# Performance work log

Measured on AMD Instinct MI355X. Metric: run time of the kernel, lower is better.

## Reference

```python
import jax, jax.numpy as jnp
import numpy as np

N_STEPS = 5
N_ETYPES = 4
N_GRAPHS = 64
HEADS = 2
N, E, D = 50000, 600000, 128
C = 32


def setup_inputs() -> dict:
    key = jax.random.key(0)
    ks = jax.random.split(key, 24)
    s = 0.08  # param scale to keep activations well-conditioned
    return {
        "in_feat1": jax.random.normal(ks[0], (N, D), jnp.float32),
        "in_feat2": jax.random.normal(ks[1], (N, D), jnp.float32),
        "src1": jax.random.randint(ks[2], (E,), 0, N, jnp.int32),
        "dst1": jax.random.randint(ks[3], (E,), 0, N, jnp.int32),
        "etype1": jax.random.randint(ks[4], (E,), 0, N_ETYPES, jnp.int32),
        "gid1": jnp.sort(jax.random.randint(ks[5], (N,), 0, N_GRAPHS, jnp.int32)),
        "src2": jax.random.randint(ks[6], (E,), 0, N, jnp.int32),
        "dst2": jax.random.randint(ks[7], (E,), 0, N, jnp.int32),
        "etype2": jax.random.randint(ks[8], (E,), 0, N_ETYPES, jnp.int32),
        "gid2": jnp.sort(jax.random.randint(ks[9], (N,), 0, N_GRAPHS, jnp.int32)),
        "W_et": jax.random.normal(ks[10], (N_ETYPES, D, D), jnp.float32) * s,
        "b_et": jax.random.normal(ks[11], (N_ETYPES, D), jnp.float32) * s,
        "W_ih": jax.random.normal(ks[12], (3 * D, D), jnp.float32) * s,
        "W_hh": jax.random.normal(ks[13], (3 * D, D), jnp.float32) * s,
        "b_ih": jax.random.normal(ks[14], (3 * D,), jnp.float32) * s,
        "b_hh": jax.random.normal(ks[15], (3 * D,), jnp.float32) * s,
        "W_fc": jax.random.normal(ks[16], (HEADS * D, D), jnp.float32) * s,
        "attn_l": jax.random.normal(ks[17], (HEADS, D), jnp.float32) * s,
        "attn_r": jax.random.normal(ks[18], (HEADS, D), jnp.float32) * s,
        "gat_bias": jax.random.normal(ks[19], (HEADS * D,), jnp.float32) * s,
        "W_cls": jax.random.normal(ks[20], (C, D), jnp.float32) * s,
        "b_cls": jax.random.normal(ks[21], (C,), jnp.float32) * s,
    }


def _ggann(feat, src, dst, etype, gid,
           W_et, b_et, W_ih, W_hh, b_ih, b_hh,
           W_fc, attn_l, attn_r, gat_bias, W_cls, b_cls):
    n = feat.shape[0]
    h = feat  # in_feats == out_feats -> no zero-padding needed
    # ---- GatedGraphConv: n_steps of per-etype message passing + GRU ----
    for _ in range(N_STEPS):
        # per-etype linear on all nodes: [K, N, D]
        t = jnp.einsum('kod,nd->kno', W_et, h) + b_et[:, None, :]
        msg = t[etype, src]                         # [E, D] gather by (etype, src)
        a = jax.ops.segment_sum(msg, dst, num_segments=n)  # [N, D]
        # GRUCell(a, h)
        gi = a @ W_ih.T + b_ih                      # [N, 3D]
        gh = h @ W_hh.T + b_hh
        i_r, i_z, i_n = jnp.split(gi, 3, axis=1)
        h_r, h_z, h_n = jnp.split(gh, 3, axis=1)
        r = jax.nn.sigmoid(i_r + h_r)
        z = jax.nn.sigmoid(i_z + h_z)
        nn_ = jnp.tanh(i_n + r * h_n)
        h = (1.0 - z) * nn_ + z * h
    # F.normalize (L2 over dim=1) then sigmoid
    h = h / jnp.maximum(jnp.linalg.norm(h, axis=1, keepdims=True), 1e-12)
    h = jax.nn.sigmoid(h)
    # ---- GATConv (num_heads=2) ----
    zft = (h @ W_fc.T).reshape(n, HEADS, D)         # [N, H, D]
    el = jnp.sum(zft * attn_l[None], axis=-1)       # [N, H]
    er = jnp.sum(zft * attn_r[None], axis=-1)
    e = jax.nn.leaky_relu(el[src] + er[dst], 0.2)   # [E, H]
    m = jax.ops.segment_max(e, dst, num_segments=n)
    ex = jnp.exp(e - m[dst])
    den = jax.ops.segment_sum(ex, dst, num_segments=n)
    alpha = ex / den[dst]                           # edge softmax per dst, per head
    rst = jax.ops.segment_sum(alpha[:, :, None] * zft[src], dst, num_segments=n)
    rst = rst + gat_bias.reshape(1, HEADS, D)
    h = jax.nn.relu(rst)                            # [N, H, D] (dropout = eval identity)
    # ---- mean_nodes per graph + classify ----
    sums = jax.ops.segment_sum(h, gid, num_segments=N_GRAPHS)      # [B, H, D]
    cnt = jax.ops.segment_sum(jnp.ones((n, 1, 1), h.dtype), gid, num_segments=N_GRAPHS)
    hg = sums / jnp.maximum(cnt, 1.0)
    return hg @ W_cls.T + b_cls                     # [B, H, C]


def reference(in_feat1, in_feat2, src1, dst1, etype1, gid1,
              src2, dst2, etype2, gid2,
              W_et, b_et, W_ih, W_hh, b_ih, b_hh,
              W_fc, attn_l, attn_r, gat_bias, W_cls, b_cls):
    params = (W_et, b_et, W_ih, W_hh, b_ih, b_hh,
              W_fc, attn_l, attn_r, gat_bias, W_cls, b_cls)
    h1 = _ggann(in_feat1, src1, dst1, etype1, gid1, *params)  # [B, H, C]
    h2 = _ggann(in_feat2, src2, dst2, etype2, gid2, *params)
    # F.pairwise_distance(p=2, eps=1e-6) over last dim -> [B, H]
    dist = jnp.linalg.norm(h1 - h2 + 1e-6, axis=-1)
    return jax.nn.softmax(dist, axis=1)             # softmax over the 2 heads
```

## Files before the change

kernel.cpp:

```cpp
#include <hip/hip_runtime.h>
#include <math.h>

#define D 128
#define NG 64
#define NG2 128
#define NSTEPS 5

using short8 = __attribute__((ext_vector_type(8))) short;
using f32x4  = __attribute__((ext_vector_type(4))) float;
using f32x2  = __attribute__((ext_vector_type(2))) float;

__device__ __forceinline__ float sigf(float x) {
  float e = __expf(-fabsf(x));
  float inv = __fdividef(1.f, 1.f + e);
  return x >= 0.f ? inv : e * inv;
}
__device__ __forceinline__ float tanhf_fast(float x) {
  float e = __expf(-2.f * fabsf(x));
  float r = (1.f - e) * __fdividef(1.f, 1.f + e);
  return x >= 0.f ? r : -r;
}
__device__ __forceinline__ float lrelu(float x) { return x > 0.f ? x : 0.2f * x; }
__device__ __forceinline__ short f2bf(float x) {
  unsigned u = __float_as_uint(x);
  u += 0x7fff + ((u >> 16) & 1);
  return (short)(u >> 16);
}
__device__ __forceinline__ unsigned pk2(float x, float y) {
  return ((unsigned)(unsigned short)f2bf(y) << 16) | (unsigned short)f2bf(x);
}
__device__ __forceinline__ float bflo(unsigned v) { return __uint_as_float(v << 16); }
__device__ __forceinline__ float bfhi(unsigned v) { return __uint_as_float(v & 0xffff0000u); }
__device__ __forceinline__ float bf2f(short s) {
  return __uint_as_float(((unsigned)(unsigned short)s) << 16);
}
__device__ __forceinline__ unsigned char f2fp8(float x) {
  int p = __builtin_amdgcn_cvt_pk_fp8_f32(x, x, 0, false);
  return (unsigned char)(p & 0xff);
}

__global__ void k_init(const float* __restrict__ f1, const float* __restrict__ f2,
                       short* __restrict__ hb, int Nd4) {
  int tot = 2 * Nd4;
  for (int i = blockIdx.x * blockDim.x + threadIdx.x; i < tot; i += gridDim.x * blockDim.x) {
    float4 v = (i < Nd4) ? ((const float4*)f1)[i] : ((const float4*)f2)[i - Nd4];
    ((uint2*)hb)[i] = make_uint2(pk2(v.x, v.y), pk2(v.z, v.w));
  }
}

__global__ void k_pack(const float* __restrict__ W, short* __restrict__ P, int NC) {
  int n = NC * 128;
  for (int i = blockIdx.x * blockDim.x + threadIdx.x; i < n; i += gridDim.x * blockDim.x) {
    int j = i & 7;
    int lane = (i >> 3) & 63;
    int kt = (i >> 9) & 3;
    int nt = i >> 11;
    int c = nt * 16 + (lane & 15);
    int k = kt * 32 + ((lane >> 4) << 3) + j;
    P[i] = f2bf(W[c * 128 + k]);
  }
}

__global__ void k_packA512(const float* __restrict__ W_et, short* __restrict__ P) {
  int n = 128 * 512;
  for (int i = blockIdx.x * blockDim.x + threadIdx.x; i < n; i += gridDim.x * blockDim.x) {
    int j = i & 7;
    int lane = (i >> 3) & 63;
    int kt = (i >> 9) & 15;
    int nt = i >> 13;
    int c = nt * 16 + (lane & 15);
    int k = kt * 32 + ((lane >> 4) << 3) + j;
    P[i] = f2bf(W_et[(k >> 7) * 16384 + c * 128 + (k & 127)]);
  }
}

__global__ void k_hist(const int* __restrict__ dst1, const int* __restrict__ dst2,
                       int E, int N, int* __restrict__ deg) {
  for (int e = blockIdx.x * blockDim.x + threadIdx.x; e < 2 * E; e += gridDim.x * blockDim.x) {
    int d = (e < E) ? dst1[e] : dst2[e - E] + N;
    atomicAdd(&deg[d], 1);
  }
}

__global__ __launch_bounds__(256) void k_scan_a(const int* __restrict__ deg, int n,
                                                int* __restrict__ bsum) {
  int base = blockIdx.x * 1024 + threadIdx.x * 4;
  int s = 0;
  if (base + 3 < n) {
    int4 v = *(const int4*)(deg + base);
    s = v.x + v.y + v.z + v.w;
  } else {
    for (int k = 0; k < 4; ++k) if (base + k < n) s += deg[base + k];
  }
  #pragma unroll
  for (int off = 32; off; off >>= 1) s += __shfl_xor(s, off);
  __shared__ int ws[4];
  if ((threadIdx.x & 63) == 0) ws[threadIdx.x >> 6] = s;
  __syncthreads();
  if (threadIdx.x == 0) bsum[blockIdx.x] = ws[0] + ws[1] + ws[2] + ws[3];
}

__global__ __launch_bounds__(1024) void k_scan_b(const int* __restrict__ bsum,
                                                 int* __restrict__ boffs, int nb) {
  int tid = threadIdx.x;
  int v = (tid < nb) ? bsum[tid] : 0;
  int lane = tid & 63, wv = tid >> 6;
  int x = v;
  #pragma unroll
  for (int off = 1; off < 64; off <<= 1) {
    int y = __shfl_up(x, off);
    if (lane >= off) x += y;
  }
  __shared__ int wsum[16];
  if (lane == 63) wsum[wv] = x;
  __syncthreads();
  if (tid < 16) {
    int u = wsum[tid];
    #pragma unroll
    for (int off = 1; off < 16; off <<= 1) {
      int y = __shfl_up(u, off);
      if (tid >= off) u += y;
    }
    wsum[tid] = u;
  }
  __syncthreads();
  int woff = wv ? wsum[wv - 1] : 0;
  if (tid < nb) boffs[tid] = woff + x - v;
}

__global__ __launch_bounds__(256) void k_scan_c(const int* __restrict__ deg,
    const int* __restrict__ boffs, int* __restrict__ row_ofs,
    int* __restrict__ cursor, int n) {
  int base = blockIdx.x * 1024 + threadIdx.x * 4;
  int v[4] = {0, 0, 0, 0};
  if (base + 3 < n) {
    int4 t = *(const int4*)(deg + base);
    v[0] = t.x; v[1] = t.y; v[2] = t.z; v[3] = t.w;
  } else {
    for (int k = 0; k < 4; ++k) if (base + k < n) v[k] = deg[base + k];
  }
  int s = v[0] + v[1] + v[2] + v[3];
  int lane = threadIdx.x & 63, wv = threadIdx.x >> 6;
  int x = s;
  #pragma unroll
  for (int off = 1; off < 64; off <<= 1) {
    int y = __shfl_up(x, off);
    if (lane >= off) x += y;
  }
  __shared__ int wsum[4];
  if (lane == 63) wsum[wv] = x;
  __syncthreads();
  int woff = 0;
  for (int w = 0; w < wv; ++w) woff += wsum[w];
  int run = boffs[blockIdx.x] + woff + x - s;
  #pragma unroll
  for (int k = 0; k < 4; ++k) {
    int i = base + k;
    if (i < n) {
      cursor[i] = run;
      run += v[k];
      row_ofs[i + 1] = run;
    }
  }
  if (blockIdx.x == 0 && threadIdx.x == 0) row_ofs[0] = 0;
}

__global__ void k_scatter(const int* __restrict__ src1, const int* __restrict__ dst1,
                          const int* __restrict__ ety1, const int* __restrict__ src2,
                          const int* __restrict__ dst2, const int* __restrict__ ety2,
                          int E, int N, int* __restrict__ cursor,
                          int* __restrict__ csr_se) {
  for (int e = blockIdx.x * blockDim.x + threadIdx.x; e < 2 * E; e += gridDim.x * blockDim.x) {
    int s, d, et;
    if (e < E) { s = src1[e]; d = dst1[e]; et = ety1[e]; }
    else { s = src2[e - E] + N; d = dst2[e - E] + N; et = ety2[e - E]; }
    int p = atomicAdd(&cursor[d], 1);
    csr_se[p] = s * 4 + et;
  }
}

__global__ void k_fillgid(const int* __restrict__ gid1, const int* __restrict__ gid2,
                          int N, int* __restrict__ gidc, int* __restrict__ gcnt) {
  __shared__ int cnt[NG2];
  int t = threadIdx.x;
  if (t < NG2) cnt[t] = 0;
  __syncthreads();
  int i = blockIdx.x * 256 + t;
  if (i < 2 * N) {
    int g = (i < N) ? gid1[i] : gid2[i - N] + NG;
    gidc[i] = g;
    atomicAdd(&cnt[g], 1);
  }
  __syncthreads();
  if (t < NG2 && cnt[t]) atomicAdd(&gcnt[t], cnt[t]);
}

__global__ __launch_bounds__(1024) void k_aggemm(const short* __restrict__ hb,
    const int* __restrict__ row_ofs, const int* __restrict__ csr_se,
    const short* __restrict__ WaP, const float* __restrict__ b_et,
    short* __restrict__ ab, int M) {
  __shared__ short Stile[16 * 512];
  __shared__ float lcnt[16][4];
  int tid = threadIdx.x;
  int lane = tid & 63, wave = tid >> 6;
  int row0 = blockIdx.x * 16;

  int li = wave;
  int node = row0 + li;
  float a0x = 0.f, a0y = 0.f, a1x = 0.f, a1y = 0.f;
  float a2x = 0.f, a2y = 0.f, a3x = 0.f, a3y = 0.f;
  int c0 = 0, c1 = 0, c2 = 0, c3 = 0;
  if (node < M) {
    int beg = row_ofs[node], end = row_ofs[node + 1];
    #define ACC(ET, VX, VY) do { \
        if (ET == 0)      { a0x += VX; a0y += VY; ++c0; } \
        else if (ET == 1) { a1x += VX; a1y += VY; ++c1; } \
        else if (ET == 2) { a2x += VX; a2y += VY; ++c2; } \
        else              { a3x += VX; a3y += VY; ++c3; } } while (0)
    for (int base = beg; base < end; base += 64) {
      int nv = end - base; if (nv > 64) nv = 64;
      int r = (lane < nv) ? csr_se[base + lane] : 0;
      int j = 0;
      for (; j + 8 <= nv; j += 8) {
        int rr0 = __builtin_amdgcn_readlane(r, j + 0);
        int rr1 = __builtin_amdgcn_readlane(r, j + 1);
        int rr2 = __builtin_amdgcn_readlane(r, j + 2);
        int rr3 = __builtin_amdgcn_readlane(r, j + 3);
        int rr4 = __builtin_amdgcn_readlane(r, j + 4);
        int rr5 = __builtin_amdgcn_readlane(r, j + 5);
        int rr6 = __builtin_amdgcn_readlane(r, j + 6);
        int rr7 = __builtin_amdgcn_readlane(r, j + 7);
        unsigned v0 = ((const unsigned*)(hb + (size_t)(rr0 >> 2) * 128))[lane];
        unsigned v1 = ((const unsigned*)(hb + (size_t)(rr1 >> 2) * 128))[lane];
        unsigned v2 = ((const unsigned*)(hb + (size_t)(rr2 >> 2) * 128))[lane];
        unsigned v3 = ((const unsigned*)(hb + (size_t)(rr3 >> 2) * 128))[lane];
        unsigned v4 = ((const unsigned*)(hb + (size_t)(rr4 >> 2) * 128))[lane];
        unsigned v5 = ((const unsigned*)(hb + (size_t)(rr5 >> 2) * 128))[lane];
        unsigned v6 = ((const unsigned*)(hb + (size_t)(rr6 >> 2) * 128))[lane];
        unsigned v7 = ((const unsigned*)(hb + (size_t)(rr7 >> 2) * 128))[lane];
        ACC(rr0 & 3, bflo(v0), bfhi(v0));
        ACC(rr1 & 3, bflo(v1), bfhi(v1));
        ACC(rr2 & 3, bflo(v2), bfhi(v2));
        ACC(rr3 & 3, bflo(v3), bfhi(v3));
        ACC(rr4 & 3, bflo(v4), bfhi(v4));
        ACC(rr5 & 3, bflo(v5), bfhi(v5));
        ACC(rr6 & 3, bflo(v6), bfhi(v6));
        ACC(rr7 & 3, bflo(v7), bfhi(v7));
      }
      for (; j + 4 <= nv; j += 4) {
        int rr0 = __builtin_amdgcn_readlane(r, j + 0);
        int rr1 = __builtin_amdgcn_readlane(r, j + 1);
        int rr2 = __builtin_amdgcn_readlane(r, j + 2);
        int rr3 = __builtin_amdgcn_readlane(r, j + 3);
        unsigned v0 = ((const unsigned*)(hb + (size_t)(rr0 >> 2) * 128))[lane];
        unsigned v1 = ((const unsigned*)(hb + (size_t)(rr1 >> 2) * 128))[lane];
        unsigned v2 = ((const unsigned*)(hb + (size_t)(rr2 >> 2) * 128))[lane];
        unsigned v3 = ((const unsigned*)(hb + (size_t)(rr3 >> 2) * 128))[lane];
        ACC(rr0 & 3, bflo(v0), bfhi(v0));
        ACC(rr1 & 3, bflo(v1), bfhi(v1));
        ACC(rr2 & 3, bflo(v2), bfhi(v2));
        ACC(rr3 & 3, bflo(v3), bfhi(v3));
      }
      for (; j < nv; ++j) {
        int rr = __builtin_amdgcn_readlane(r, j);
        unsigned v = ((const unsigned*)(hb + (size_t)(rr >> 2) * 128))[lane];
        ACC(rr & 3, bflo(v), bfhi(v));
      }
    }
    #undef ACC
  }
  {
    int swz = (li & 7) << 4;
    unsigned* ld = (unsigned*)Stile;
    ld[(li * 1024 + ((lane * 4      ) ^ swz)) >> 2] = pk2(a0x, a0y);
    ld[(li * 1024 + ((lane * 4 + 256) ^ swz)) >> 2] = pk2(a1x, a1y);
    ld[(li * 1024 + ((lane * 4 + 512) ^ swz)) >> 2] = pk2(a2x, a2y);
    ld[(li * 1024 + ((lane * 4 + 768) ^ swz)) >> 2] = pk2(a3x, a3y);
    if (lane == 0) {
      lcnt[li][0] = (float)c0; lcnt[li][1] = (float)c1;
      lcnt[li][2] = (float)c2; lcnt[li][3] = (float)c3;
    }
  }
  __syncthreads();

  if (wave < 8) {
    int quad = lane >> 4, l15 = lane & 15;
    int swz = (l15 & 7) << 4;
    int nt = wave;
    f32x4 acc = {0.f, 0.f, 0.f, 0.f};
    #pragma unroll
    for (int kt = 0; kt < 16; ++kt) {
      int boff = l15 * 1024 + ((kt * 64 + quad * 16) ^ swz);
      short8 a = *(const short8*)((const char*)Stile + boff);
      short8 b = *(const short8*)(WaP + (((size_t)(nt * 16 + kt) * 64) + lane) * 8);
      acc = __builtin_amdgcn_mfma_f32_16x16x32_bf16(a, b, acc, 0, 0, 0);
    }
    int c = nt * 16 + l15;
    float be0 = b_et[c], be1 = b_et[128 + c], be2 = b_et[256 + c], be3 = b_et[384 + c];
    #pragma unroll
    for (int reg = 0; reg < 4; ++reg) {
      int lr = quad * 4 + reg;
      int r = row0 + lr;
      if (r < M) {
        float v = acc[reg] + lcnt[lr][0] * be0 + lcnt[lr][1] * be1
                           + lcnt[lr][2] * be2 + lcnt[lr][3] * be3;
        ab[(size_t)r * 128 + c] = f2bf(v);
      }
    }
  }
}

__global__ __launch_bounds__(256) void k_gru_mfma(const short* __restrict__ ab,
    short* __restrict__ hb,
    const short* __restrict__ Pih, const short* __restrict__ Phh,
    const float* __restrict__ b_ih, const float* __restrict__ b_hh, int M) {
  int tid = threadIdx.x;
  int lane = tid & 63, wave = tid >> 6;
  int row0 = blockIdx.x * 128 + wave * 32;
  int quad = lane >> 4, l15 = lane & 15;
  short8 fa[2][4], fh[2][4];
  #pragma unroll
  for (int rt = 0; rt < 2; ++rt) {
    int ar = row0 + rt * 16 + l15; if (ar >= M) ar = M - 1;
    #pragma unroll
    for (int kt = 0; kt < 4; ++kt) {
      fa[rt][kt] = *(const short8*)(ab + (size_t)ar * 128 + kt * 32 + quad * 8);
      fh[rt][kt] = *(const short8*)(hb + (size_t)ar * 128 + kt * 32 + quad * 8);
    }
  }
  for (int nt = 0; nt < 8; ++nt) {
    f32x4 accr[2], accz[2], acci[2], acch[2];
    #pragma unroll
    for (int rt = 0; rt < 2; ++rt) {
      accr[rt] = {0.f,0.f,0.f,0.f}; accz[rt] = {0.f,0.f,0.f,0.f};
      acci[rt] = {0.f,0.f,0.f,0.f}; acch[rt] = {0.f,0.f,0.f,0.f};
    }
    #pragma unroll
    for (int kt = 0; kt < 4; ++kt) {
      size_t li = ((size_t)lane) * 8;
      short8 wr = *(const short8*)(Pih + ((size_t)((nt     ) * 4 + kt) * 64) * 8 + li);
      short8 wz = *(const short8*)(Pih + ((size_t)((nt +  8) * 4 + kt) * 64) * 8 + li);
      short8 wn = *(const short8*)(Pih + ((size_t)((nt + 16) * 4 + kt) * 64) * 8 + li);
      short8 ur = *(const short8*)(Phh + ((size_t)((nt     ) * 4 + kt) * 64) * 8 + li);
      short8 uz = *(const short8*)(Phh + ((size_t)((nt +  8) * 4 + kt) * 64) * 8 + li);
      short8 un = *(const short8*)(Phh + ((size_t)((nt + 16) * 4 + kt) * 64) * 8 + li);
      #pragma unroll
      for (int rt = 0; rt < 2; ++rt) {
        accr[rt] = __builtin_amdgcn_mfma_f32_16x16x32_bf16(fa[rt][kt], wr, accr[rt], 0, 0, 0);
        accr[rt] = __builtin_amdgcn_mfma_f32_16x16x32_bf16(fh[rt][kt], ur, accr[rt], 0, 0, 0);
        accz[rt] = __builtin_amdgcn_mfma_f32_16x16x32_bf16(fa[rt][kt], wz, accz[rt], 0, 0, 0);
        accz[rt] = __builtin_amdgcn_mfma_f32_16x16x32_bf16(fh[rt][kt], uz, accz[rt], 0, 0, 0);
        acci[rt] = __builtin_amdgcn_mfma_f32_16x16x32_bf16(fa[rt][kt], wn, acci[rt], 0, 0, 0);
        acch[rt] = __builtin_amdgcn_mfma_f32_16x16x32_bf16(fh[rt][kt], un, acch[rt], 0, 0, 0);
      }
    }
    int c = nt * 16 + l15;
    float bir = b_ih[c],      bhr = b_hh[c];
    float biz = b_ih[c+128],  bhz = b_hh[c+128];
    float bin_= b_ih[c+256],  bhn = b_hh[c+256];
    #pragma unroll
    for (int rt = 0; rt < 2; ++rt) {
      #pragma unroll
      for (int reg = 0; reg < 4; ++reg) {
        int r = row0 + rt * 16 + quad * 4 + reg;
        if (r < M) {
          float rg = sigf(accr[rt][reg] + bir + bhr);
          float zg = sigf(accz[rt][reg] + biz + bhz);
          float ng = tanhf_fast(acci[rt][reg] + bin_ + rg * (acch[rt][reg] + bhn));
          float hold = bf2f(hb[(size_t)r * 128 + c]);
          float hn2 = (1.f - zg) * ng + zg * hold;
          hb[(size_t)r * 128 + c] = f2bf(hn2);
        }
      }
    }
  }
}

__global__ __launch_bounds__(256) void k_fc_eler(const short* __restrict__ Ab,
    const short* __restrict__ Bp, const float* __restrict__ attn_l,
    const float* __restrict__ attn_r, unsigned char* __restrict__ zq,
    float* __restrict__ el, float* __restrict__ er, int M) {
  int tid = threadIdx.x;
  int lane = tid & 63, wave = tid >> 6;
  int row0 = blockIdx.x * 128 + wave * 32;
  int quad = lane >> 4, l15 = lane & 15;
  short8 af[2][4];
  #pragma unroll
  for (int rt = 0; rt < 2; ++rt) {
    int ar = row0 + rt * 16 + l15; if (ar >= M) ar = M - 1;
    #pragma unroll
    for (int kt = 0; kt < 4; ++kt)
      af[rt][kt] = *(const short8*)(Ab + (size_t)ar * 128 + kt * 32 + quad * 8);
  }
  #pragma unroll
  for (int rt = 0; rt < 2; ++rt) {
    float ss = 0.f;
    #pragma unroll
    for (int kt = 0; kt < 4; ++kt)
      #pragma unroll
      for (int j = 0; j < 8; ++j) {
        float x = bf2f(af[rt][kt][j]);
        ss += x * x;
      }
    ss += __shfl_xor(ss, 16);
    ss += __shfl_xor(ss, 32);
    float inv = 1.f / fmaxf(sqrtf(ss), 1e-12f);
    #pragma unroll
    for (int kt = 0; kt < 4; ++kt)
      #pragma unroll
      for (int j = 0; j < 8; ++j)
        af[rt][kt][j] = f2bf(sigf(bf2f(af[rt][kt][j]) * inv));
  }
  float elp[2][2][4] = {};
  float erp[2][2][4] = {};
  for (int nt = 0; nt < 16; ++nt) {
    f32x4 a0 = {0.f,0.f,0.f,0.f}, a1 = {0.f,0.f,0.f,0.f};
    #pragma unroll
    for (int kt = 0; kt < 4; ++kt) {
      short8 b = *(const short8*)(Bp + (((size_t)(nt * 4 + kt) * 64) + lane) * 8);
      a0 = __builtin_amdgcn_mfma_f32_16x16x32_bf16(af[0][kt], b, a0, 0, 0, 0);
      a1 = __builtin_amdgcn_mfma_f32_16x16x32_bf16(af[1][kt], b, a1, 0, 0, 0);
    }
    int head = nt >> 3;
    int colh = (nt & 7) * 16 + l15;
    float alv = attn_l[head * 128 + colh];
    float arv = attn_r[head * 128 + colh];
    int c = nt * 16 + l15;
    #pragma unroll
    for (int rt = 0; rt < 2; ++rt) {
      f32x4 acc = rt ? a1 : a0;
      #pragma unroll
      for (int reg = 0; reg < 4; ++reg) {
        int r = row0 + rt * 16 + quad * 4 + reg;
        if (r < M) zq[(size_t)r * 256 + c] = f2fp8(acc[reg]);
        elp[rt][head][reg] += acc[reg] * alv;
        erp[rt][head][reg] += acc[reg] * arv;
      }
    }
  }
  #pragma unroll
  for (int off = 1; off < 16; off <<= 1) {
    #pragma unroll
    for (int rt = 0; rt < 2; ++rt)
      #pragma unroll
      for (int h = 0; h < 2; ++h)
        #pragma unroll
        for (int reg = 0; reg < 4; ++reg) {
          elp[rt][h][reg] += __shfl_xor(elp[rt][h][reg], off);
          erp[rt][h][reg] += __shfl_xor(erp[rt][h][reg], off);
        }
  }
  if (l15 == 0) {
    #pragma unroll
    for (int rt = 0; rt < 2; ++rt)
      #pragma unroll
      for (int h = 0; h < 2; ++h)
        #pragma unroll
        for (int reg = 0; reg < 4; ++reg) {
          int r = row0 + rt * 16 + quad * 4 + reg;
          if (r < M) {
            el[r * 2 + h] = elp[rt][h][reg];
            er[r * 2 + h] = erp[rt][h][reg];
          }
        }
  }
}

__global__ __launch_bounds__(256) void k_gat(const unsigned char* __restrict__ zq,
    const float* __restrict__ el, const float* __restrict__ er,
    const int* __restrict__ row_ofs, const int* __restrict__ csr_se,
    const float* __restrict__ gat_bias, short* __restrict__ outb, int N) {
  int node = blockIdx.x * 4 + (threadIdx.x >> 6);
  int lane = threadIdx.x & 63;
  if (node >= N) return;
  int beg = row_ofs[node], end = row_ofs[node + 1];
  float2 ern = ((const float2*)er)[node];
  float l0 = 0.f, l1 = 0.f;
  float4 acc = {0.f, 0.f, 0.f, 0.f};
  int head = lane >> 5;
  for (int base = beg; base < end; base += 64) {
    int nv = end - base; if (nv > 64) nv = 64;
    int sidx = (lane < nv) ? (csr_se[base + lane] >> 2) : 0;
    float p0 = 0.f, p1 = 0.f;
    if (lane < nv) {
      float2 els = ((const float2*)el)[sidx];
      p0 = expf(lrelu(els.x + ern.x));
      p1 = expf(lrelu(els.y + ern.y));
    }
    float t0 = p0, t1 = p1;
    #pragma unroll
    for (int off = 32; off; off >>= 1) { t0 += __shfl_xor(t0, off); t1 += __shfl_xor(t1, off); }
    l0 += t0; l1 += t1;
    int w01 = (int)pk2(p0, p1);
    int j = 0;
    for (; j + 4 <= nv; j += 4) {
      int s0 = __builtin_amdgcn_readlane(sidx, j + 0);
      int s1 = __builtin_amdgcn_readlane(sidx, j + 1);
      int s2 = __builtin_amdgcn_readlane(sidx, j + 2);
      int s3 = __builtin_amdgcn_readlane(sidx, j + 3);
      unsigned w0 = (unsigned)__builtin_amdgcn_readlane(w01, j + 0);
      unsigned w1 = (unsigned)__builtin_amdgcn_readlane(w01, j + 1);
      unsigned w2 = (unsigned)__builtin_amdgcn_readlane(w01, j + 2);
      unsigned w3 = (unsigned)__builtin_amdgcn_readlane(w01, j + 3);
      unsigned z0 = ((const unsigned*)(zq + (size_t)s0 * 256))[lane];
      unsigned z1 = ((const unsigned*)(zq + (size_t)s1 * 256))[lane];
      unsigned z2 = ((const unsigned*)(zq + (size_t)s2 * 256))[lane];
      unsigned z3 = ((const unsigned*)(zq + (size_t)s3 * 256))[lane];
      float f0 = head ? bfhi(w0) : bflo(w0);
      float f1 = head ? bfhi(w1) : bflo(w1);
      float f2 = head ? bfhi(w2) : bflo(w2);
      float f3 = head ? bfhi(w3) : bflo(w3);
      f32x2 lo, hi;
      lo = __builtin_amdgcn_cvt_pk_f32_fp8(z0, false);
      hi = __builtin_amdgcn_cvt_pk_f32_fp8(z0, true);
      acc.x += f0 * lo[0]; acc.y += f0 * lo[1]; acc.z += f0 * hi[0]; acc.w += f0 * hi[1];
      lo = __builtin_amdgcn_cvt_pk_f32_fp8(z1, false);
      hi = __builtin_amdgcn_cvt_pk_f32_fp8(z1, true);
      acc.x += f1 * lo[0]; acc.y += f1 * lo[1]; acc.z += f1 * hi[0]; acc.w += f1 * hi[1];
      lo = __builtin_amdgcn_cvt_pk_f32_fp8(z2, false);
      hi = __builtin_amdgcn_cvt_pk_f32_fp8(z2, true);
      acc.x += f2 * lo[0]; acc.y += f2 * lo[1]; acc.z += f2 * hi[0]; acc.w += f2 * hi[1];
      lo = __builtin_amdgcn_cvt_pk_f32_fp8(z3, false);
      hi = __builtin_amdgcn_cvt_pk_f32_fp8(z3, true);
      acc.x += f3 * lo[0]; acc.y += f3 * lo[1]; acc.z += f3 * hi[0]; acc.w += f3 * hi[1];
    }
    for (; j < nv; ++j) {
      int sj = __builtin_amdgcn_readlane(sidx, j);
      unsigned wj = (unsigned)__builtin_amdgcn_readlane(w01, j);
      float w = head ? bfhi(wj) : bflo(wj);
      unsigned zv = ((const unsigned*)(zq + (size_t)sj * 256))[lane];
      f32x2 lo = __builtin_amdgcn_cvt_pk_f32_fp8(zv, false);
      f32x2 hi = __builtin_amdgcn_cvt_pk_f32_fp8(zv, true);
      acc.x += w * lo[0]; acc.y += w * lo[1];
      acc.z += w * hi[0]; acc.w += w * hi[1];
    }
  }
  float inv0 = (l0 > 0.f) ? 1.f / l0 : 0.f;
  float inv1 = (l1 > 0.f) ? 1.f / l1 : 0.f;
  float inv = head ? inv1 : inv0;
  float4 b = ((const float4*)gat_bias)[lane];
  float ox = fmaxf(acc.x * inv + b.x, 0.f);
  float oy = fmaxf(acc.y * inv + b.y, 0.f);
  float oz = fmaxf(acc.z * inv + b.z, 0.f);
  float ow = fmaxf(acc.w * inv + b.w, 0.f);
  ((uint2*)(outb + (size_t)node * 256))[lane] = make_uint2(pk2(ox, oy), pk2(oz, ow));
}

__global__ __launch_bounds__(256) void k_segred(const short* __restrict__ hgatb,
    const int* __restrict__ gidc, float* __restrict__ sums, int NT2) {
  int node0 = blockIdx.x * 128;
  int col = threadIdx.x;
  int end = node0 + 128; if (end > NT2) end = NT2;
  if (node0 >= NT2) return;
  float acc = 0.f;
  int gcur = gidc[node0];
  for (int n = node0; n < end; ++n) {
    int g = gidc[n];
    if (g != gcur) {
      atomicAdd(&sums[gcur * 256 + col], acc);
      acc = 0.f; gcur = g;
    }
    acc += bf2f(hgatb[(size_t)n * 256 + col]);
  }
  atomicAdd(&sums[gcur * 256 + col], acc);
}

__global__ __launch_bounds__(64) void k_classify(const float* __restrict__ sums,
    const int* __restrict__ gcnt, const float* __restrict__ W_cls,
    const float* __restrict__ b_cls, float* __restrict__ logits) {
  int g = blockIdx.x, tid = threadIdx.x;
  int hh = tid >> 5, c = tid & 31;
  float invc = 1.f / fmaxf((float)gcnt[g], 1.f);
  float acc = 0.f;
  for (int d = 0; d < D; ++d)
    acc += (sums[g * 256 + hh * D + d] * invc) * W_cls[c * D + d];
  logits[g * 64 + hh * 32 + c] = acc + b_cls[c];
}

__global__ __launch_bounds__(64) void k_final(const float* __restrict__ logits,
    float* __restrict__ out) {
  int g = threadIdx.x;
  if (g >= NG) return;
  float d[2];
  #pragma unroll
  for (int hh = 0; hh < 2; ++hh) {
    float s = 0.f;
    for (int c = 0; c < 32; ++c) {
      float df = logits[g * 64 + hh * 32 + c] - logits[(g + NG) * 64 + hh * 32 + c] + 1e-6f;
      s += df * df;
    }
    d[hh] = sqrtf(s);
  }
  float mx = fmaxf(d[0], d[1]);
  float e0 = expf(d[0] - mx), e1 = expf(d[1] - mx);
  float den = e0 + e1;
  out[g * 2] = e0 / den;
  out[g * 2 + 1] = e1 / den;
}

extern "C" void kernel_launch(void* const* d_in, const int* in_sizes, int n_in,
                              void* d_out, int out_size, void* d_ws, size_t ws_size,
                              hipStream_t stream) {
  const float* in_feat1 = (const float*)d_in[0];
  const float* in_feat2 = (const float*)d_in[1];
  const int* src1 = (const int*)d_in[2];
  const int* dst1 = (const int*)d_in[3];
  const int* ety1 = (const int*)d_in[4];
  const int* gid1 = (const int*)d_in[5];
  const int* src2 = (const int*)d_in[6];
  const int* dst2 = (const int*)d_in[7];
  const int* ety2 = (const int*)d_in[8];
  const int* gid2 = (const int*)d_in[9];
  const float* W_et = (const float*)d_in[10];
  const float* b_et = (const float*)d_in[11];
  const float* W_ih = (const float*)d_in[12];
  const float* W_hh = (const float*)d_in[13];
  const float* b_ih = (const float*)d_in[14];
  const float* b_hh = (const float*)d_in[15];
  const float* W_fc = (const float*)d_in[16];
  const float* attn_l = (const float*)d_in[17];
  const float* attn_r = (const float*)d_in[18];
  const float* gat_bias = (const float*)d_in[19];
  const float* W_cls = (const float*)d_in[20];
  const float* b_cls = (const float*)d_in[21];
  float* out = (float*)d_out;

  int N = in_sizes[0] / D;
  int E = in_sizes[2];
  int N2 = 2 * N, E2 = 2 * E;

  char* p = (char*)d_ws;
  auto alloc = [&](size_t bytes) -> void* {
    char* r = p;
    p += (bytes + 255) & ~(size_t)255;
    return (void*)r;
  };
  short* WaP  = (short*)alloc((size_t)512 * 128 * 2);
  short* WihP = (short*)alloc((size_t)384 * 128 * 2);
  short* WhhP = (short*)alloc((size_t)384 * 128 * 2);
  short* WfcP = (short*)alloc((size_t)256 * 128 * 2);
  short* hb  = (short*)alloc((size_t)N2 * D * 2);
  short* ab  = (short*)alloc((size_t)N2 * D * 2);
  short* hgatb = (short*)alloc((size_t)N2 * 256 * 2);
  unsigned char* zq = (unsigned char*)alloc((size_t)N2 * 256);
  float* el  = (float*)alloc((size_t)N2 * 2 * 4);
  float* er  = (float*)alloc((size_t)N2 * 2 * 4);
  float* sums= (float*)alloc((size_t)NG2 * 256 * 4);
  float* logits = (float*)alloc((size_t)NG2 * 64 * 4);
  int* deg     = (int*)alloc((size_t)N2 * 4);
  int* row_ofs = (int*)alloc(((size_t)N2 + 1) * 4);
  int* cursor  = (int*)alloc((size_t)N2 * 4);
  int* gidc    = (int*)alloc((size_t)N2 * 4);
  int* gcnt    = (int*)alloc((size_t)NG2 * 4);
  int* bsum    = (int*)alloc((size_t)1024 * 4);
  int* boffs   = (int*)alloc((size_t)1024 * 4);
  int* csr_se  = (int*)alloc((size_t)E2 * 4);
  if ((size_t)(p - (char*)d_ws) > ws_size) return;

  k_packA512<<<dim3(32), dim3(256), 0, stream>>>(W_et, WaP);
  k_pack<<<dim3(48), dim3(256), 0, stream>>>(W_ih, WihP, 384);
  k_pack<<<dim3(48), dim3(256), 0, stream>>>(W_hh, WhhP, 384);
  k_pack<<<dim3(32), dim3(256), 0, stream>>>(W_fc, WfcP, 256);

  hipMemsetAsync(deg, 0, (size_t)N2 * 4, stream);
  hipMemsetAsync(gcnt, 0, (size_t)NG2 * 4, stream);
  int eb = (E2 + 255) / 256;
  int nb = (N2 + 1023) / 1024;
  k_hist<<<dim3(eb), dim3(256), 0, stream>>>(dst1, dst2, E, N, deg);
  k_scan_a<<<dim3(nb), dim3(256), 0, stream>>>(deg, N2, bsum);
  k_scan_b<<<dim3(1), dim3(1024), 0, stream>>>(bsum, boffs, nb);
  k_scan_c<<<dim3(nb), dim3(256), 0, stream>>>(deg, boffs, row_ofs, cursor, N2);
  k_scatter<<<dim3(eb), dim3(256), 0, stream>>>(src1, dst1, ety1, src2, dst2, ety2,
                                                E, N, cursor, csr_se);
  k_fillgid<<<dim3((N2 + 255) / 256), dim3(256), 0, stream>>>(gid1, gid2, N, gidc, gcnt);

  k_init<<<dim3(1024), dim3(256), 0, stream>>>(in_feat1, in_feat2, hb, N * D / 4);

  int gb16 = (N2 + 15) / 16;
  int gb128 = (N2 + 127) / 128;
  int nb4 = (N2 + 3) / 4;

  for (int s = 0; s < NSTEPS; ++s) {
    k_aggemm<<<dim3(gb16), dim3(1024), 0, stream>>>(hb, row_ofs, csr_se, WaP, b_et, ab, N2);
    k_gru_mfma<<<dim3(gb128), dim3(256), 0, stream>>>(ab, hb, WihP, WhhP, b_ih, b_hh, N2);
  }
  k_fc_eler<<<dim3(gb128), dim3(256), 0, stream>>>(hb, WfcP, attn_l, attn_r, zq, el, er, N2);
  k_gat<<<dim3(nb4), dim3(256), 0, stream>>>(zq, el, er, row_ofs, csr_se,
                                             gat_bias, hgatb, N2);
  hipMemsetAsync(sums, 0, (size_t)NG2 * 256 * 4, stream);
  k_segred<<<dim3((N2 + 127) / 128), dim3(256), 0, stream>>>(hgatb, gidc, sums, N2);
  k_classify<<<dim3(NG2), dim3(64), 0, stream>>>(sums, gcnt, W_cls, b_cls, logits);
  k_final<<<dim3(1), dim3(64), 0, stream>>>(logits, out);
}
```

Before: 1.199 ms.

## Fuse setup, histogram, and classify kernels; pre-scale CSR indices to byte offsets

Merges the weight-packing kernels, the memsets and the input bf16 conversion into one grid-stride setup kernel, and merges the histogram with the gid fill, cutting the launch count. The sums memset moves into k_gat, and classify plus final softmax become a single one-block kernel. CSR entries now store the source index shifted so it doubles as a byte offset, which removes multiplies from the gather address computation. The single-block classify serializes more work, and the 22-bit source field caps node count near 4M.

```diff
diff --git a/kernel.cpp b/kernel.cpp
--- a/kernel.cpp
+++ b/kernel.cpp
@@ -39,46 +39,82 @@
   return (unsigned char)(p & 0xff);
 }
 
-__global__ void k_init(const float* __restrict__ f1, const float* __restrict__ f2,
-                       short* __restrict__ hb, int Nd4) {
-  int tot = 2 * Nd4;
-  for (int i = blockIdx.x * blockDim.x + threadIdx.x; i < tot; i += gridDim.x * blockDim.x) {
-    float4 v = (i < Nd4) ? ((const float4*)f1)[i] : ((const float4*)f2)[i - Nd4];
-    ((uint2*)hb)[i] = make_uint2(pk2(v.x, v.y), pk2(v.z, v.w));
-  }
-}
-
-__global__ void k_pack(const float* __restrict__ W, short* __restrict__ P, int NC) {
-  int n = NC * 128;
-  for (int i = blockIdx.x * blockDim.x + threadIdx.x; i < n; i += gridDim.x * blockDim.x) {
-    int j = i & 7;
-    int lane = (i >> 3) & 63;
-    int kt = (i >> 9) & 3;
-    int nt = i >> 11;
-    int c = nt * 16 + (lane & 15);
-    int k = kt * 32 + ((lane >> 4) << 3) + j;
-    P[i] = f2bf(W[c * 128 + k]);
-  }
-}
-
-__global__ void k_packA512(const float* __restrict__ W_et, short* __restrict__ P) {
-  int n = 128 * 512;
-  for (int i = blockIdx.x * blockDim.x + threadIdx.x; i < n; i += gridDim.x * blockDim.x) {
-    int j = i & 7;
-    int lane = (i >> 3) & 63;
-    int kt = (i >> 9) & 15;
-    int nt = i >> 13;
-    int c = nt * 16 + (lane & 15);
-    int k = kt * 32 + ((lane >> 4) << 3) + j;
-    P[i] = f2bf(W_et[(k >> 7) * 16384 + c * 128 + (k & 127)]);
-  }
-}
-
-__global__ void k_hist(const int* __restrict__ dst1, const int* __restrict__ dst2,
-                       int E, int N, int* __restrict__ deg) {
-  for (int e = blockIdx.x * blockDim.x + threadIdx.x; e < 2 * E; e += gridDim.x * blockDim.x) {
-    int d = (e < E) ? dst1[e] : dst2[e - E] + N;
-    atomicAdd(&deg[d], 1);
+__device__ __forceinline__ void packK128(const float* __restrict__ W,
+                                         short* __restrict__ P, int i) {
+  int j = i & 7;
+  int lane = (i >> 3) & 63;
+  int kt = (i >> 9) & 3;
+  int nt = i >> 11;
+  int c = nt * 16 + (lane & 15);
+  int k = kt * 32 + ((lane >> 4) << 3) + j;
+  P[i] = f2bf(W[c * 128 + k]);
+}
+__device__ __forceinline__ void packA512f(const float* __restrict__ W_et,
+                                          short* __restrict__ P, int i) {
+  int j = i & 7;
+  int lane = (i >> 3) & 63;
+  int kt = (i >> 9) & 15;
+  int nt = i >> 13;
+  int c = nt * 16 + (lane & 15);
+  int k = kt * 32 + ((lane >> 4) << 3) + j;
+  P[i] = f2bf(W_et[(k >> 7) * 16384 + c * 128 + (k & 127)]);
+}
+
+__global__ __launch_bounds__(256) void k_setup(const float* __restrict__ W_et,
+    const float* __restrict__ W_ih, const float* __restrict__ W_hh,
+    const float* __restrict__ W_fc, const float* __restrict__ f1,
+    const float* __restrict__ f2, short* __restrict__ WaP, short* __restrict__ WihP,
+    short* __restrict__ WhhP, short* __restrict__ WfcP, short* __restrict__ hb,
+    int* __restrict__ deg, int* __restrict__ gcnt, int N2, int Nd4) {
+  const int sA = 65536, sB = 49152, sC = 49152, sD = 32768;
+  int sE = N2, sF = NG2;
+  long sG = 2L * Nd4;
+  long tot = (long)(sA + sB + sC + sD) + sE + sF + sG;
+  for (long ii = (long)blockIdx.x * blockDim.x + threadIdx.x; ii < tot;
+       ii += (long)gridDim.x * blockDim.x) {
+    long r = ii;
+    if (r < sA) { packA512f(W_et, WaP, (int)r); continue; }
+    r -= sA;
+    if (r < sB) { packK128(W_ih, WihP, (int)r); continue; }
+    r -= sB;
+    if (r < sC) { packK128(W_hh, WhhP, (int)r); continue; }
+    r -= sC;
+    if (r < sD) { packK128(W_fc, WfcP, (int)r); continue; }
+    r -= sD;
+    if (r < sE) { deg[r] = 0; continue; }
+    r -= sE;
+    if (r < sF) { gcnt[r] = 0; continue; }
+    r -= sF;
+    {
+      int i = (int)r;
+      float4 v = (i < Nd4) ? ((const float4*)f1)[i] : ((const float4*)f2)[i - Nd4];
+      ((uint2*)hb)[i] = make_uint2(pk2(v.x, v.y), pk2(v.z, v.w));
+    }
+  }
+}
+
+__global__ __launch_bounds__(256) void k_histgid(const int* __restrict__ dst1,
+    const int* __restrict__ dst2, const int* __restrict__ gid1,
+    const int* __restrict__ gid2, int E, int N, int* __restrict__ deg,
+    int* __restrict__ gidc, int* __restrict__ gcnt, int EB) {
+  __shared__ int cnt[NG2];
+  if ((int)blockIdx.x < EB) {
+    for (int e = blockIdx.x * 256 + threadIdx.x; e < 2 * E; e += EB * 256) {
+      int d = (e < E) ? dst1[e] : dst2[e - E] + N;
+      atomicAdd(&deg[d], 1);
+    }
+  } else {
+    int t = threadIdx.x;
+    if (t < NG2) cnt[t] = 0;
+    __syncthreads();
+    int i = (blockIdx.x - EB) * 256 + t;
+    if (i < 2 * N) {
+      int g = (i < N) ? gid1[i] : gid2[i - N] + NG;
+      gidc[i] = g;
+      atomicAdd(&cnt[g], 1);
+    }
+    __syncthreads();
+    if (t < NG2 && cnt[t]) atomicAdd(&gcnt[t], cnt[t]);
   }
 }
 
@@ -175,24 +211,8 @@
     if (e < E) { s = src1[e]; d = dst1[e]; et = ety1[e]; }
     else { s = src2[e - E] + N; d = dst2[e - E] + N; et = ety2[e - E]; }
     int p = atomicAdd(&cursor[d], 1);
-    csr_se[p] = s * 4 + et;
-  }
-}
-
-__global__ void k_fillgid(const int* __restrict__ gid1, const int* __restrict__ gid2,
-                          int N, int* __restrict__ gidc, int* __restrict__ gcnt) {
-  __shared__ int cnt[NG2];
-  int t = threadIdx.x;
-  if (t < NG2) cnt[t] = 0;
-  __syncthreads();
-  int i = blockIdx.x * 256 + t;
-  if (i < 2 * N) {
-    int g = (i < N) ? gid1[i] : gid2[i - N] + NG;
-    gidc[i] = g;
-    atomicAdd(&cnt[g], 1);
-  }
-  __syncthreads();
-  if (t < NG2 && cnt[t]) atomicAdd(&gcnt[t], cnt[t]);
+    csr_se[p] = (s << 10) + et;
+  }
 }
 
 __global__ __launch_bounds__(1024) void k_aggemm(const short* __restrict__ hb,
@@ -207,16 +227,16 @@
 
   int li = wave;
   int node = row0 + li;
-  float a0x = 0.f, a0y = 0.f, a1x = 0.f, a1y = 0.f;
-  float a2x = 0.f, a2y = 0.f, a3x = 0.f, a3y = 0.f;
+  f32x2 A0 = {0.f, 0.f}, A1 = {0.f, 0.f}, A2 = {0.f, 0.f}, A3 = {0.f, 0.f};
   int c0 = 0, c1 = 0, c2 = 0, c3 = 0;
+  const char* hbb = (const char*)hb;
   if (node < M) {
     int beg = row_ofs[node], end = row_ofs[node + 1];
-    #define ACC(ET, VX, VY) do { \
-        if (ET == 0)      { a0x += VX; a0y += VY; ++c0; } \
-        else if (ET == 1) { a1x += VX; a1y += VY; ++c1; } \
-        else if (ET == 2) { a2x += VX; a2y += VY; ++c2; } \
-        else              { a3x += VX; a3y += VY; ++c3; } } while (0)
+    #define ACC(ET, V) do { f32x2 t_; t_[0] = bflo(V); t_[1] = bfhi(V); \
+        if (ET == 0)      { A0 += t_; ++c0; } \
+        else if (ET == 1) { A1 += t_; ++c1; } \
+        else if (ET == 2) { A2 += t_; ++c2; } \
+        else              { A3 += t_; ++c3; } } while (0)
     for (int base = beg; base < end; base += 64) {
       int nv = end - base; if (nv > 64) nv = 64;
       int r = (lane < nv) ? csr_se[base + lane] : 0;
@@ -230,41 +250,41 @@
         int rr5 = __builtin_amdgcn_readlane(r, j + 5);
         int rr6 = __builtin_amdgcn_readlane(r, j + 6);
         int rr7 = __builtin_amdgcn_readlane(r, j + 7);
-        unsigned v0 = ((const unsigned*)(hb + (size_t)(rr0 >> 2) * 128))[lane];
-        unsigned v1 = ((const unsigned*)(hb + (size_t)(rr1 >> 2) * 128))[lane];
-        unsigned v2 = ((const unsigned*)(hb + (size_t)(rr2 >> 2) * 128))[lane];
-        unsigned v3 = ((const unsigned*)(hb + (size_t)(rr3 >> 2) * 128))[lane];
-        unsigned v4 = ((const unsigned*)(hb + (size_t)(rr4 >> 2) * 128))[lane];
-        unsigned v5 = ((const unsigned*)(hb + (size_t)(rr5 >> 2) * 128))[lane];
-        unsigned v6 = ((const unsigned*)(hb + (size_t)(rr6 >> 2) * 128))[lane];
-        unsigned v7 = ((const unsigned*)(hb + (size_t)(rr7 >> 2) * 128))[lane];
-        ACC(rr0 & 3, bflo(v0), bfhi(v0));
-        ACC(rr1 & 3, bflo(v1), bfhi(v1));
-        ACC(rr2 & 3, bflo(v2), bfhi(v2));
-        ACC(rr3 & 3, bflo(v3), bfhi(v3));
-        ACC(rr4 & 3, bflo(v4), bfhi(v4));
-        ACC(rr5 & 3, bflo(v5), bfhi(v5));
-        ACC(rr6 & 3, bflo(v6), bfhi(v6));
-        ACC(rr7 & 3, bflo(v7), bfhi(v7));
+        unsigned v0 = ((const unsigned*)(hbb + (rr0 >> 2)))[lane];
+        unsigned v1 = ((const unsigned*)(hbb + (rr1 >> 2)))[lane];
+        unsigned v2 = ((const unsigned*)(hbb + (rr2 >> 2)))[lane];
+        unsigned v3 = ((const unsigned*)(hbb + (rr3 >> 2)))[lane];
+        unsigned v4 = ((const unsigned*)(hbb + (rr4 >> 2)))[lane];
+        unsigned v5 = ((const unsigned*)(hbb + (rr5 >> 2)))[lane];
+        unsigned v6 = ((const unsigned*)(hbb + (rr6 >> 2)))[lane];
+        unsigned v7 = ((const unsigned*)(hbb + (rr7 >> 2)))[lane];
+        ACC(rr0 & 3, v0);
+        ACC(rr1 & 3, v1);
+        ACC(rr2 & 3, v2);
+        ACC(rr3 & 3, v3);
+        ACC(rr4 & 3, v4);
+        ACC(rr5 & 3, v5);
+        ACC(rr6 & 3, v6);
+        ACC(rr7 & 3, v7);
       }
       for (; j + 4 <= nv; j += 4) {
         int rr0 = __builtin_amdgcn_readlane(r, j + 0);
         int rr1 = __builtin_amdgcn_readlane(r, j + 1);
         int rr2 = __builtin_amdgcn_readlane(r, j + 2);
         int rr3 = __builtin_amdgcn_readlane(r, j + 3);
-        unsigned v0 = ((const unsigned*)(hb + (size_t)(rr0 >> 2) * 128))[lane];
-        unsigned v1 = ((const unsigned*)(hb + (size_t)(rr1 >> 2) * 128))[lane];
-        unsigned v2 = ((const unsigned*)(hb + (size_t)(rr2 >> 2) * 128))[lane];
-        unsigned v3 = ((const unsigned*)(hb + (size_t)(rr3 >> 2) * 128))[lane];
-        ACC(rr0 & 3, bflo(v0), bfhi(v0));
-        ACC(rr1 & 3, bflo(v1), bfhi(v1));
-        ACC(rr2 & 3, bflo(v2), bfhi(v2));
-        ACC(rr3 & 3, bflo(v3), bfhi(v3));
+        unsigned v0 = ((const unsigned*)(hbb + (rr0 >> 2)))[lane];
+        unsigned v1 = ((const unsigned*)(hbb + (rr1 >> 2)))[lane];
+        unsigned v2 = ((const unsigned*)(hbb + (rr2 >> 2)))[lane];
+        unsigned v3 = ((const unsigned*)(hbb + (rr3 >> 2)))[lane];
+        ACC(rr0 & 3, v0);
+        ACC(rr1 & 3, v1);
+        ACC(rr2 & 3, v2);
+        ACC(rr3 & 3, v3);
       }
       for (; j < nv; ++j) {
         int rr = __builtin_amdgcn_readlane(r, j);
-        unsigned v = ((const unsigned*)(hb + (size_t)(rr >> 2) * 128))[lane];
-        ACC(rr & 3, bflo(v), bfhi(v));
+        unsigned v = ((const unsigned*)(hbb + (rr >> 2)))[lane];
+        ACC(rr & 3, v);
       }
     }
     #undef ACC
@@ -272,10 +292,10 @@
   {
     int swz = (li & 7) << 4;
     unsigned* ld = (unsigned*)Stile;
-    ld[(li * 1024 + ((lane * 4      ) ^ swz)) >> 2] = pk2(a0x, a0y);
-    ld[(li * 1024 + ((lane * 4 + 256) ^ swz)) >> 2] = pk2(a1x, a1y);
-    ld[(li * 1024 + ((lane * 4 + 512) ^ swz)) >> 2] = pk2(a2x, a2y);
-    ld[(li * 1024 + ((lane * 4 + 768) ^ swz)) >> 2] = pk2(a3x, a3y);
+    ld[(li * 1024 + ((lane * 4      ) ^ swz)) >> 2] = pk2(A0[0], A0[1]);
+    ld[(li * 1024 + ((lane * 4 + 256) ^ swz)) >> 2] = pk2(A1[0], A1[1]);
+    ld[(li * 1024 + ((lane * 4 + 512) ^ swz)) >> 2] = pk2(A2[0], A2[1]);
+    ld[(li * 1024 + ((lane * 4 + 768) ^ swz)) >> 2] = pk2(A3[0], A3[1]);
     if (lane == 0) {
       lcnt[li][0] = (float)c0; lcnt[li][1] = (float)c1;
       lcnt[li][2] = (float)c2; lcnt[li][3] = (float)c3;
@@ -469,7 +489,9 @@
 __global__ __launch_bounds__(256) void k_gat(const unsigned char* __restrict__ zq,
     const float* __restrict__ el, const float* __restrict__ er,
     const int* __restrict__ row_ofs, const int* __restrict__ csr_se,
-    const float* __restrict__ gat_bias, short* __restrict__ outb, int N) {
+    const float* __restrict__ gat_bias, short* __restrict__ outb,
+    float* __restrict__ sums, int N) {
+  if (blockIdx.x < NG2) sums[blockIdx.x * 256 + threadIdx.x] = 0.f;
   int node = blockIdx.x * 4 + (threadIdx.x >> 6);
   int lane = threadIdx.x & 63;
   if (node >= N) return;
@@ -478,12 +500,14 @@
   float l0 = 0.f, l1 = 0.f;
   float4 acc = {0.f, 0.f, 0.f, 0.f};
   int head = lane >> 5;
+  const char* elb = (const char*)el;
+  const char* zqb = (const char*)zq;
   for (int base = beg; base < end; base += 64) {
     int nv = end - base; if (nv > 64) nv = 64;
-    int sidx = (lane < nv) ? (csr_se[base + lane] >> 2) : 0;
+    int se = (lane < nv) ? csr_se[base + lane] : 0;
     float p0 = 0.f, p1 = 0.f;
     if (lane < nv) {
-      float2 els = ((const float2*)el)[sidx];
+      float2 els = *(const float2*)(elb + (se >> 7));
       p0 = expf(lrelu(els.x + ern.x));
       p1 = expf(lrelu(els.y + ern.y));
     }
@@ -494,18 +518,18 @@
     int w01 = (int)pk2(p0, p1);
     int j = 0;
     for (; j + 4 <= nv; j += 4) {
-      int s0 = __builtin_amdgcn_readlane(sidx, j + 0);
-      int s1 = __builtin_amdgcn_readlane(sidx, j + 1);
-      int s2 = __builtin_amdgcn_readlane(sidx, j + 2);
-      int s3 = __builtin_amdgcn_readlane(sidx, j + 3);
+      int b0 = __builtin_amdgcn_readlane(se, j + 0) >> 2;
+      int b1 = __builtin_amdgcn_readlane(se, j + 1) >> 2;
+      int b2 = __builtin_amdgcn_readlane(se, j + 2) >> 2;
+      int b3 = __builtin_amdgcn_readlane(se, j + 3) >> 2;
       unsigned w0 = (unsigned)__builtin_amdgcn_readlane(w01, j + 0);
       unsigned w1 = (unsigned)__builtin_amdgcn_readlane(w01, j + 1);
       unsigned w2 = (unsigned)__builtin_amdgcn_readlane(w01, j + 2);
       unsigned w3 = (unsigned)__builtin_amdgcn_readlane(w01, j + 3);
-      unsigned z0 = ((const unsigned*)(zq + (size_t)s0 * 256))[lane];
-      unsigned z1 = ((const unsigned*)(zq + (size_t)s1 * 256))[lane];
-      unsigned z2 = ((const unsigned*)(zq + (size_t)s2 * 256))[lane];
-      unsigned z3 = ((const unsigned*)(zq + (size_t)s3 * 256))[lane];
+      unsigned z0 = ((const unsigned*)(zqb + b0))[lane];
+      unsigned z1 = ((const unsigned*)(zqb + b1))[lane];
+      unsigned z2 = ((const unsigned*)(zqb + b2))[lane];
+      unsigned z3 = ((const unsigned*)(zqb + b3))[lane];
       float f0 = head ? bfhi(w0) : bflo(w0);
       float f1 = head ? bfhi(w1) : bflo(w1);
       float f2 = head ? bfhi(w2) : bflo(w2);
@@ -525,10 +549,10 @@
       acc.x += f3 * lo[0]; acc.y += f3 * lo[1]; acc.z += f3 * hi[0]; acc.w += f3 * hi[1];
     }
     for (; j < nv; ++j) {
-      int sj = __builtin_amdgcn_readlane(sidx, j);
+      int bj = __builtin_amdgcn_readlane(se, j) >> 2;
       unsigned wj = (unsigned)__builtin_amdgcn_readlane(w01, j);
       float w = head ? bfhi(wj) : bflo(wj);
-      unsigned zv = ((const unsigned*)(zq + (size_t)sj * 256))[lane];
+      unsigned zv = ((const unsigned*)(zqb + bj))[lane];
       f32x2 lo = __builtin_amdgcn_cvt_pk_f32_fp8(zv, false);
       f32x2 hi = __builtin_amdgcn_cvt_pk_f32_fp8(zv, true);
       acc.x += w * lo[0]; acc.y += w * lo[1];
@@ -565,37 +589,39 @@
   atomicAdd(&sums[gcur * 256 + col], acc);
 }
 
-__global__ __launch_bounds__(64) void k_classify(const float* __restrict__ sums,
+__global__ __launch_bounds__(1024) void k_classfin(const float* __restrict__ sums,
     const int* __restrict__ gcnt, const float* __restrict__ W_cls,
-    const float* __restrict__ b_cls, float* __restrict__ logits) {
-  int g = blockIdx.x, tid = threadIdx.x;
-  int hh = tid >> 5, c = tid & 31;
-  float invc = 1.f / fmaxf((float)gcnt[g], 1.f);
-  float acc = 0.f;
-  for (int d = 0; d < D; ++d)
-    acc += (sums[g * 256 + hh * D + d] * invc) * W_cls[c * D + d];
-  logits[g * 64 + hh * 32 + c] = acc + b_cls[c];
-}
-
-__global__ __launch_bounds__(64) void k_final(const float* __restrict__ logits,
-    float* __restrict__ out) {
-  int g = threadIdx.x;
-  if (g >= NG) return;
-  float d[2];
-  #pragma unroll
-  for (int hh = 0; hh < 2; ++hh) {
-    float s = 0.f;
-    for (int c = 0; c < 32; ++c) {
-      float df = logits[g * 64 + hh * 32 + c] - logits[(g + NG) * 64 + hh * 32 + c] + 1e-6f;
-      s += df * df;
-    }
-    d[hh] = sqrtf(s);
-  }
-  float mx = fmaxf(d[0], d[1]);
-  float e0 = expf(d[0] - mx), e1 = expf(d[1] - mx);
-  float den = e0 + e1;
-  out[g * 2] = e0 / den;
-  out[g * 2 + 1] = e1 / den;
+    const float* __restrict__ b_cls, float* __restrict__ out) {
+  __shared__ float lg[NG2 * 64];
+  int tid = threadIdx.x;
+  for (int o = tid; o < NG2 * 64; o += 1024) {
+    int g = o >> 6, hh = (o >> 5) & 1, c = o & 31;
+    float invc = 1.f / fmaxf((float)gcnt[g], 1.f);
+    const float* sp = sums + g * 256 + hh * D;
+    const float* wp = W_cls + c * D;
+    float acc = 0.f;
+    for (int d = 0; d < D; ++d) acc += sp[d] * wp[d];
+    lg[o] = acc * invc + b_cls[c];
+  }
+  __syncthreads();
+  if (tid < NG) {
+    int g = tid;
+    float dd[2];
+    #pragma unroll
+    for (int hh = 0; hh < 2; ++hh) {
+      float s = 0.f;
+      for (int c = 0; c < 32; ++c) {
+        float df = lg[g * 64 + hh * 32 + c] - lg[(g + NG) * 64 + hh * 32 + c] + 1e-6f;
+        s += df * df;
+      }
+      dd[hh] = sqrtf(s);
+    }
+    float mx = fmaxf(dd[0], dd[1]);
+    float e0 = expf(dd[0] - mx), e1 = expf(dd[1] - mx);
+    float den = e0 + e1;
+    out[g * 2] = e0 / den;
+    out[g * 2 + 1] = e1 / den;
+  }
 }
 
 extern "C" void kernel_launch(void* const* d_in, const int* in_sizes, int n_in,
@@ -646,7 +672,6 @@
   float* el  = (float*)alloc((size_t)N2 * 2 * 4);
   float* er  = (float*)alloc((size_t)N2 * 2 * 4);
   float* sums= (float*)alloc((size_t)NG2 * 256 * 4);
-  float* logits = (float*)alloc((size_t)NG2 * 64 * 4);
   int* deg     = (int*)alloc((size_t)N2 * 4);
   int* row_ofs = (int*)alloc(((size_t)N2 + 1) * 4);
   int* cursor  = (int*)alloc((size_t)N2 * 4);
@@ -657,24 +682,19 @@
   int* csr_se  = (int*)alloc((size_t)E2 * 4);
   if ((size_t)(p - (char*)d_ws) > ws_size) return;
 
-  k_packA512<<<dim3(32), dim3(256), 0, stream>>>(W_et, WaP);
-  k_pack<<<dim3(48), dim3(256), 0, stream>>>(W_ih, WihP, 384);
-  k_pack<<<dim3(48), dim3(256), 0, stream>>>(W_hh, WhhP, 384);
-  k_pack<<<dim3(32), dim3(256), 0, stream>>>(W_fc, WfcP, 256);
-
-  hipMemsetAsync(deg, 0, (size_t)N2 * 4, stream);
-  hipMemsetAsync(gcnt, 0, (size_t)NG2 * 4, stream);
-  int eb = (E2 + 255) / 256;
+  k_setup<<<dim3(2048), dim3(256), 0, stream>>>(W_et, W_ih, W_hh, W_fc,
+      in_feat1, in_feat2, WaP, WihP, WhhP, WfcP, hb, deg, gcnt, N2, N * D / 4);
+
+  int EB = (E2 + 255) / 256;
+  int GB = (N2 + 255) / 256;
   int nb = (N2 + 1023) / 1024;
-  k_hist<<<dim3(eb), dim3(256), 0, stream>>>(dst1, dst2, E, N, deg);
+  k_histgid<<<dim3(EB + GB), dim3(256), 0, stream>>>(dst1, dst2, gid1, gid2,
+                                                     E, N, deg, gidc, gcnt, EB);
   k_scan_a<<<dim3(nb), dim3(256), 0, stream>>>(deg, N2, bsum);
   k_scan_b<<<dim3(1), dim3(1024), 0, stream>>>(bsum, boffs, nb);
   k_scan_c<<<dim3(nb), dim3(256), 0, stream>>>(deg, boffs, row_ofs, cursor, N2);
-  k_scatter<<<dim3(eb), dim3(256), 0, stream>>>(src1, dst1, ety1, src2, dst2, ety2,
+  k_scatter<<<dim3(EB), dim3(256), 0, stream>>>(src1, dst1, ety1, src2, dst2, ety2,
                                                 E, N, cursor, csr_se);
-  k_fillgid<<<dim3((N2 + 255) / 256), dim3(256), 0, stream>>>(gid1, gid2, N, gidc, gcnt);
-
-  k_init<<<dim3(1024), dim3(256), 0, stream>>>(in_feat1, in_feat2, hb, N * D / 4);
 
   int gb16 = (N2 + 15) / 16;
   int gb128 = (N2 + 127) / 128;
@@ -686,9 +706,7 @@
   }
   k_fc_eler<<<dim3(gb128), dim3(256), 0, stream>>>(hb, WfcP, attn_l, attn_r, zq, el, er, N2);
   k_gat<<<dim3(nb4), dim3(256), 0, stream>>>(zq, el, er, row_ofs, csr_se,
-                                             gat_bias, hgatb, N2);
-  hipMemsetAsync(sums, 0, (size_t)NG2 * 256 * 4, stream);
+                                             gat_bias, hgatb, sums, N2);
   k_segred<<<dim3((N2 + 127) / 128), dim3(256), 0, stream>>>(hgatb, gidc, sums, N2);
-  k_classify<<<dim3(NG2), dim3(64), 0, stream>>>(sums, gcnt, W_cls, b_cls, logits);
-  k_final<<<dim3(1), dim3(64), 0, stream>>>(logits, out);
-}
+  k_classfin<<<dim3(1), dim3(1024), 0, stream>>>(sums, gcnt, W_cls, b_cls, out);
+}
```

Measured after the change: 1.293 ms. 1.08x slower.
